# Optimization experiments

Hardware: AMD Instinct MI355X
Metric: run time of the kernel (lower is better)

Reference implementation:

```python
import jax, jax.numpy as jnp
import numpy as np

D_MODEL = 1024
N_HEAD = 16
ATT_DIM = D_MODEL // N_HEAD


def setup_inputs() -> dict:
    key = jax.random.key(0)
    ks = jax.random.split(key, 7)
    B, S = 2, 2048
    q = jax.random.normal(ks[0], (B, S, D_MODEL), dtype=jnp.float32)
    k = jax.random.normal(ks[1], (B, S, D_MODEL), dtype=jnp.float32)
    v = jax.random.normal(ks[2], (B, S, D_MODEL), dtype=jnp.float32)
    # per-head projection weights, stored as [H, d_model, att_dim] (x @ W form)
    scale_qkv = float(np.sqrt(6.0 / (D_MODEL + ATT_DIM)))  # xavier_uniform
    Wq = jax.random.uniform(ks[3], (N_HEAD, D_MODEL, ATT_DIM), jnp.float32, -scale_qkv, scale_qkv)
    Wk = jax.random.uniform(ks[4], (N_HEAD, D_MODEL, ATT_DIM), jnp.float32, -scale_qkv, scale_qkv)
    Wv = jax.random.uniform(ks[5], (N_HEAD, D_MODEL, ATT_DIM), jnp.float32, -scale_qkv, scale_qkv)
    scale_o = float(np.sqrt(6.0 / (D_MODEL + D_MODEL)))
    Wo = jax.random.uniform(ks[6], (D_MODEL, D_MODEL), jnp.float32, -scale_o, scale_o)
    return {"q": q, "k": k, "v": v, "Wq": Wq, "Wk": Wk, "Wv": Wv, "Wo": Wo}


def reference(q, k, v, Wq, Wk, Wv, Wo):
    # per-head projections, batched over heads: [H,B,S,E]
    qh = jnp.einsum('bsd,hde->hbse', q, Wq)
    kh = jnp.einsum('bsd,hde->hbse', k, Wk)
    vh = jnp.einsum('bsd,hde->hbse', v, Wv)
    # NOTE: original divides by att_dim (not sqrt(att_dim))
    scores = jnp.einsum('hbqe,hbke->hbqk', qh, kh) / ATT_DIM
    attn = jax.nn.softmax(scores, axis=-1)  # [H,B,Sq,Sk]
    att = jnp.einsum('hbqk,hbke->hbqe', attn, vh)  # [H,B,S,E]
    # concat heads along last dim in head order, then output projection
    H, B, S, E = att.shape
    cat = jnp.transpose(att, (1, 2, 0, 3)).reshape(B, S, H * E)
    out = cat @ Wo  # dropout is identity in eval
    return (out, attn)
```

## Files before the change

### kernel.cpp

```cpp
#include <hip/hip_runtime.h>
#include <hip/hip_bf16.h>

#define DM 1024
#define NH 16
#define AD 64
#define BB 2
#define SS 2048
#define LOG2E 1.44269504f

typedef float f32x4 __attribute__((ext_vector_type(4)));
typedef short bf16x8 __attribute__((ext_vector_type(8)));
typedef unsigned short u16;
typedef unsigned int u32;
typedef u16 u16x4 __attribute__((ext_vector_type(4)));
typedef u16 u16x8 __attribute__((ext_vector_type(8)));
typedef u32 u32x4 __attribute__((ext_vector_type(4)));

static __device__ __forceinline__ u16 f2bf(float f) {
  unsigned u = __builtin_bit_cast(unsigned, f);
  u += 0x7fffu + ((u >> 16) & 1u);
  return (u16)(u >> 16);
}

#define MFMA16(a, b, c) __builtin_amdgcn_mfma_f32_16x16x32_bf16((a), (b), (c), 0, 0, 0)

static __device__ __forceinline__ void ld_lds16(const void* g, void* l) {
  __builtin_amdgcn_global_load_lds((const __attribute__((address_space(1))) u32*)g,
                                   (__attribute__((address_space(3))) u32*)l, 16, 0, 0);
}

#define KFRAG(buf, row, P) (*(const bf16x8*)(&(buf)[(row) * 64 + ((((P) ^ ((row) & 7))) << 3)]))
#define V64(buf, row, P, hh) \
  (*(const u16x4*)(&(buf)[(row) * 64 + ((((P) ^ ((row) & 7))) << 3) + (hh) * 4]))

__global__ __launch_bounds__(256, 4) void cast_bf16_kernel(const float* __restrict__ src,
                                                           u16* __restrict__ dst, int n8) {
  int i = blockIdx.x * blockDim.x + threadIdx.x;
  int stride = gridDim.x * blockDim.x;
  for (; i < n8; i += stride) {
    const f32x4* p = (const f32x4*)src + 2 * (size_t)i;
    f32x4 a = p[0], b = p[1];
    u16x8 o;
    o[0] = f2bf(a[0]); o[1] = f2bf(a[1]); o[2] = f2bf(a[2]); o[3] = f2bf(a[3]);
    o[4] = f2bf(b[0]); o[5] = f2bf(b[1]); o[6] = f2bf(b[2]); o[7] = f2bf(b[3]);
    *((u16x8*)dst + i) = o;
  }
}

__global__ __launch_bounds__(256, 4) void tcast_kernel(const float* __restrict__ src,
                                                       u16* __restrict__ dst, int R, int C,
                                                       float scale) {
  __shared__ float T[64][65];
  long bo = (long)blockIdx.z * R * C;
  int r0 = blockIdx.x * 64, c0 = blockIdx.y * 64;
  int cl = threadIdx.x & 63, rl = threadIdx.x >> 6;
#pragma unroll
  for (int i = 0; i < 16; i++) {
    int rr = rl + 4 * i;
    T[cl][rr] = src[bo + (long)(r0 + rr) * C + c0 + cl];
  }
  __syncthreads();
#pragma unroll
  for (int i = 0; i < 16; i++) {
    int cc = rl + 4 * i;
    dst[bo + (long)(c0 + cc) * R + r0 + cl] = f2bf(T[cc][cl] * scale);
  }
}

template <int MODE>
__global__ __launch_bounds__(256, 5) void proj_kernel(const u16* __restrict__ X,
                                                      const u16* __restrict__ WT,
                                                      void* __restrict__ outp, long ob, long oh,
                                                      long os, long oe) {
  __shared__ u16 Ab[2][64 * 64];
  __shared__ u16 Bb[2][64 * 64];
  int s0 = blockIdx.x * 64, h = blockIdx.y, b = blockIdx.z;
  int tid = threadIdx.x, w = tid >> 6, lane = tid & 63, g = lane >> 4, li = lane & 15;
  const u16* xb = X + ((long)b * SS + s0) * DM;
  const u16* wb = WT + (long)h * 64 * DM;
  int r1 = tid >> 3, p1 = (tid ^ (r1 & 7)) & 7;
  int r2 = (tid + 256) >> 3, p2 = ((tid + 256) ^ (r2 & 7)) & 7;
  const u16* as1 = xb + (long)r1 * DM + p1 * 8;
  const u16* as2 = xb + (long)r2 * DM + p2 * 8;
  const u16* bs1 = wb + (long)r1 * DM + p1 * 8;
  const u16* bs2 = wb + (long)r2 * DM + p2 * 8;
  u16* ad0 = &Ab[0][tid * 8]; u16* ad0b = &Ab[0][(tid + 256) * 8];
  u16* ad1 = &Ab[1][tid * 8]; u16* ad1b = &Ab[1][(tid + 256) * 8];
  u16* bd0 = &Bb[0][tid * 8]; u16* bd0b = &Bb[0][(tid + 256) * 8];
  u16* bd1 = &Bb[1][tid * 8]; u16* bd1b = &Bb[1][(tid + 256) * 8];

  ld_lds16(as1, ad0); ld_lds16(as2, ad0b);
  ld_lds16(bs1, bd0); ld_lds16(bs2, bd0b);
  asm volatile("s_waitcnt vmcnt(0)" ::: "memory");
  __syncthreads();

  f32x4 acc[4] = {};
  for (int kc = 0; kc < DM / 64; kc++) {
    if (kc + 1 < DM / 64) {
      int ko = (kc + 1) * 64;
      if (kc & 1) {
        ld_lds16(as1 + ko, ad0); ld_lds16(as2 + ko, ad0b);
        ld_lds16(bs1 + ko, bd0); ld_lds16(bs2 + ko, bd0b);
      } else {
        ld_lds16(as1 + ko, ad1); ld_lds16(as2 + ko, ad1b);
        ld_lds16(bs1 + ko, bd1); ld_lds16(bs2 + ko, bd1b);
      }
    }
    const u16* ab = Ab[kc & 1];
    const u16* bbuf = Bb[kc & 1];
    bf16x8 bf0 = KFRAG(bbuf, w * 16 + li, g);
    bf16x8 bf1 = KFRAG(bbuf, w * 16 + li, 4 + g);
#pragma unroll
    for (int mi = 0; mi < 4; mi++) {
      bf16x8 a0 = KFRAG(ab, mi * 16 + li, g);
      bf16x8 a1 = KFRAG(ab, mi * 16 + li, 4 + g);
      acc[mi] = MFMA16(a0, bf0, acc[mi]);
      acc[mi] = MFMA16(a1, bf1, acc[mi]);
    }
    asm volatile("s_waitcnt vmcnt(0)" ::: "memory");
    __syncthreads();
  }

  int e = w * 16 + li;
  long bh = (long)b * ob + (long)h * oh;
#pragma unroll
  for (int mi = 0; mi < 4; mi++) {
    int sb = s0 + mi * 16 + 4 * g;
    if (MODE == 0) {
      u16* o = (u16*)outp;
#pragma unroll
      for (int r = 0; r < 4; r++) o[bh + (long)(sb + r) * os + (long)e * oe] = f2bf(acc[mi][r]);
    } else if (MODE == 1) {
      u16x4 v;
#pragma unroll
      for (int r = 0; r < 4; r++) v[r] = f2bf(acc[mi][r]);
      *(u16x4*)((u16*)outp + bh + (long)e * oe + sb) = v;
    } else {
      float* o = (float*)outp;
#pragma unroll
      for (int r = 0; r < 4; r++) o[bh + (long)(sb + r) * os + (long)e * oe] = acc[mi][r];
    }
  }
}

__global__ __launch_bounds__(512, 4) void attn_kernel(const u16* __restrict__ qh,
                                                      const u16* __restrict__ kh,
                                                      const u16* __restrict__ vhT,
                                                      float* __restrict__ attn_out,
                                                      u16* __restrict__ cat) {
  __shared__ u16 Kb[2][64 * 64];
  __shared__ u16 Vb[2][64 * 64];
  int h = blockIdx.y, b = blockIdx.z;
  int hb = h * BB + b;
  int tid = threadIdx.x;
  int w = tid >> 6, lane = tid & 63;
  int g = lane >> 4, li = lane & 15;
  long base = (long)hb * SS * AD;
  const u16* qhb = qh + base;
  const u16* khb = kh + base;
  const u16* vhb = vhT + base;
  int q0 = blockIdx.x * 128 + w * 16;

  bf16x8 bq0 = *(const bf16x8*)(qhb + (q0 + li) * AD + 8 * g);
  bf16x8 bq1 = *(const bf16x8*)(qhb + (q0 + li) * AD + 32 + 8 * g);

  int srow = tid >> 3, spiece = (tid ^ (srow & 7)) & 7;
  const u16* ksrc = khb + (long)srow * AD + spiece * 8;
  const u16* vsrc = vhb + (long)srow * SS + spiece * 8;
  u16* kd0 = &Kb[0][tid * 8]; u16* kd1 = &Kb[1][tid * 8];
  u16* vd0 = &Vb[0][tid * 8]; u16* vd1 = &Vb[1][tid * 8];

  float m_run = -3.0e38f, l_run = 0.f;
  ld_lds16(ksrc, kd0);
  asm volatile("s_waitcnt vmcnt(0)" ::: "memory");
  __syncthreads();
  for (int ch = 0; ch < SS / 64; ch++) {
    if (ch + 1 < SS / 64) ld_lds16(ksrc + (ch + 1) * 64 * AD, (ch & 1) ? kd0 : kd1);
    const u16* kb = Kb[ch & 1];
    f32x4 sacc[4] = {};
#pragma unroll
    for (int mi = 0; mi < 4; mi++) {
      bf16x8 a0 = KFRAG(kb, mi * 16 + li, g);
      bf16x8 a1 = KFRAG(kb, mi * 16 + li, 4 + g);
      sacc[mi] = MFMA16(a0, bq0, sacc[mi]);
      sacc[mi] = MFMA16(a1, bq1, sacc[mi]);
    }
    float cm = m_run;
#pragma unroll
    for (int c = 0; c < 4; c++)
#pragma unroll
      for (int r = 0; r < 4; r++) cm = fmaxf(cm, sacc[c][r]);
    l_run *= exp2f((m_run - cm) * LOG2E);
#pragma unroll
    for (int c = 0; c < 4; c++)
#pragma unroll
      for (int r = 0; r < 4; r++) l_run += exp2f((sacc[c][r] - cm) * LOG2E);
    m_run = cm;
    asm volatile("s_waitcnt vmcnt(0)" ::: "memory");
    __syncthreads();
  }
#pragma unroll
  for (int d = 16; d <= 32; d <<= 1) {
    float om = __shfl_xor(m_run, d);
    float ol = __shfl_xor(l_run, d);
    float nm = fmaxf(m_run, om);
    l_run = l_run * exp2f((m_run - nm) * LOG2E) + ol * exp2f((om - nm) * LOG2E);
    m_run = nm;
  }
  float rinv = 1.0f / l_run;
  float mC = m_run * LOG2E;

  ld_lds16(ksrc, kd0);
  ld_lds16(vsrc, vd0);
  asm volatile("s_waitcnt vmcnt(0)" ::: "memory");
  __syncthreads();
  f32x4 accv[4] = {};
  float* arow = attn_out + ((long)hb * SS + q0 + li) * SS;
  for (int ch = 0; ch < SS / 64; ch++) {
    if (ch + 1 < SS / 64) {
      ld_lds16(ksrc + (ch + 1) * 64 * AD, (ch & 1) ? kd0 : kd1);
      ld_lds16(vsrc + (ch + 1) * 64, (ch & 1) ? vd0 : vd1);
    }
    const u16* kb = Kb[ch & 1];
    const u16* vb = Vb[ch & 1];
    f32x4 sacc[4] = {};
#pragma unroll
    for (int mi = 0; mi < 4; mi++) {
      bf16x8 a0 = KFRAG(kb, mi * 16 + li, g);
      bf16x8 a1 = KFRAG(kb, mi * 16 + li, 4 + g);
      sacc[mi] = MFMA16(a0, bq0, sacc[mi]);
      sacc[mi] = MFMA16(a1, bq1, sacc[mi]);
    }
    u32 pw[8];
#pragma unroll
    for (int c = 0; c < 4; c++) {
      f32x4 pv;
#pragma unroll
      for (int r = 0; r < 4; r++) pv[r] = exp2f(sacc[c][r] * LOG2E - mC) * rinv;
      *(f32x4*)(arow + ch * 64 + c * 16 + 4 * g) = pv;
      pw[2 * c] = (u32)f2bf(pv[0]) | ((u32)f2bf(pv[1]) << 16);
      pw[2 * c + 1] = (u32)f2bf(pv[2]) | ((u32)f2bf(pv[3]) << 16);
    }
#pragma unroll
    for (int kk = 0; kk < 2; kk++) {
      u32x4 aw = {pw[4 * kk], pw[4 * kk + 1], pw[4 * kk + 2], pw[4 * kk + 3]};
      bf16x8 ap = __builtin_bit_cast(bf16x8, aw);
#pragma unroll
      for (int et = 0; et < 4; et++) {
        int row = et * 16 + li;
        u16x4 b0 = V64(vb, row, 4 * kk + (g >> 1), g & 1);
        u16x4 b1 = V64(vb, row, 4 * kk + 2 + (g >> 1), g & 1);
        u16x8 ub = {b0[0], b0[1], b0[2], b0[3], b1[0], b1[1], b1[2], b1[3]};
        bf16x8 bv = __builtin_bit_cast(bf16x8, ub);
        accv[et] = MFMA16(ap, bv, accv[et]);
      }
    }
    asm volatile("s_waitcnt vmcnt(0)" ::: "memory");
    __syncthreads();
  }

#pragma unroll
  for (int et = 0; et < 4; et++)
#pragma unroll
    for (int r = 0; r < 4; r++)
      cat[((long)b * SS + q0 + 4 * g + r) * DM + h * AD + et * 16 + li] = f2bf(accv[et][r]);
}

extern "C" void kernel_launch(void* const* d_in, const int* in_sizes, int n_in, void* d_out,
                              int out_size, void* d_ws, size_t ws_size, hipStream_t stream) {
  const float* q = (const float*)d_in[0];
  const float* k = (const float*)d_in[1];
  const float* v = (const float*)d_in[2];
  const float* Wq = (const float*)d_in[3];
  const float* Wk = (const float*)d_in[4];
  const float* Wv = (const float*)d_in[5];
  const float* Wo = (const float*)d_in[6];
  float* out = (float*)d_out;
  float* attn_out = out + (long)BB * SS * DM;

  const long NX = (long)BB * SS * DM;
  const long NW = (long)NH * DM * AD;
  u16* ws = (u16*)d_ws;
  u16* xq = ws;
  u16* xk = xq + NX;
  u16* xv = xk + NX;
  u16* WqT = xv + NX;
  u16* WkT = WqT + NW;
  u16* WvT = WkT + NW;
  u16* WoT = WvT + NW;
  u16* qhw = WoT + (long)DM * DM;
  u16* khw = qhw + NX;
  u16* vhw = khw + NX;
  u16* catw = vhw + NX;

  cast_bf16_kernel<<<2048, 256, 0, stream>>>(q, xq, (int)(NX / 8));
  cast_bf16_kernel<<<2048, 256, 0, stream>>>(k, xk, (int)(NX / 8));
  cast_bf16_kernel<<<2048, 256, 0, stream>>>(v, xv, (int)(NX / 8));
  tcast_kernel<<<dim3(16, 1, NH), 256, 0, stream>>>(Wq, WqT, DM, AD, 1.0f / AD);
  tcast_kernel<<<dim3(16, 1, NH), 256, 0, stream>>>(Wk, WkT, DM, AD, 1.0f);
  tcast_kernel<<<dim3(16, 1, NH), 256, 0, stream>>>(Wv, WvT, DM, AD, 1.0f);
  tcast_kernel<<<dim3(16, 16, 1), 256, 0, stream>>>(Wo, WoT, DM, DM, 1.0f);

  dim3 pg(SS / 64, NH, BB);
  proj_kernel<0><<<pg, 256, 0, stream>>>(xq, WqT, qhw, (long)SS * AD, (long)BB * SS * AD, AD, 1);
  proj_kernel<0><<<pg, 256, 0, stream>>>(xk, WkT, khw, (long)SS * AD, (long)BB * SS * AD, AD, 1);
  proj_kernel<1><<<pg, 256, 0, stream>>>(xv, WvT, vhw, (long)SS * AD, (long)BB * SS * AD, 1, SS);

  attn_kernel<<<dim3(SS / 128, NH, BB), 512, 0, stream>>>(qhw, khw, vhw, attn_out, catw);

  proj_kernel<2><<<pg, 256, 0, stream>>>(catw, WoT, out, (long)SS * DM, AD, DM, 1);
}
```

Baseline: 305.3 us.

## Overlap async LDS prefetch with compute via partial vmcnt waits; merge cast launches

Replaces the full vmcnt(0) wait at the end of each loop iteration with a partial wait placed before the barrier at the top of the loop, so the next tile's global-to-LDS load stays in flight while the current tile is computed. This applies to the projection kernel and both attention passes. It also folds the softmax normalisation into the exponent offset (log2 of the row sum) and merges the three activation casts and three weight transposes into single launches to cut launch overhead. The hand-counted vmcnt values must match the number of outstanding loads, including the attn_out stores in the second attention pass, or the kernel can read stale LDS data.

```diff
diff --git a/kernel.cpp b/kernel.cpp
--- a/kernel.cpp
+++ b/kernel.cpp
@@ -29,12 +29,29 @@
                                    (__attribute__((address_space(3))) u32*)l, 16, 0, 0);
 }
 
+#define WAITV(N)                                             \
+  do {                                                       \
+    asm volatile("s_waitcnt vmcnt(" #N ")" ::: "memory");    \
+    __builtin_amdgcn_sched_barrier(0);                       \
+  } while (0)
+#define WAITL0()                                             \
+  do {                                                       \
+    asm volatile("s_waitcnt lgkmcnt(0)" ::: "memory");       \
+    __builtin_amdgcn_sched_barrier(0);                       \
+  } while (0)
+#define BAR() __builtin_amdgcn_s_barrier()
+
 #define KFRAG(buf, row, P) (*(const bf16x8*)(&(buf)[(row) * 64 + ((((P) ^ ((row) & 7))) << 3)]))
 #define V64(buf, row, P, hh) \
   (*(const u16x4*)(&(buf)[(row) * 64 + ((((P) ^ ((row) & 7))) << 3) + (hh) * 4]))
 
-__global__ __launch_bounds__(256, 4) void cast_bf16_kernel(const float* __restrict__ src,
-                                                           u16* __restrict__ dst, int n8) {
+__global__ __launch_bounds__(256, 4) void cast3_kernel(const float* __restrict__ s0,
+                                                       const float* __restrict__ s1,
+                                                       const float* __restrict__ s2,
+                                                       u16* __restrict__ d0, u16* __restrict__ d1,
+                                                       u16* __restrict__ d2, int n8) {
+  const float* src = blockIdx.y == 0 ? s0 : blockIdx.y == 1 ? s1 : s2;
+  u16* dst = blockIdx.y == 0 ? d0 : blockIdx.y == 1 ? d1 : d2;
   int i = blockIdx.x * blockDim.x + threadIdx.x;
   int stride = gridDim.x * blockDim.x;
   for (; i < n8; i += stride) {
@@ -47,11 +64,26 @@
   }
 }
 
-__global__ __launch_bounds__(256, 4) void tcast_kernel(const float* __restrict__ src,
+template <int MODE>
+__global__ __launch_bounds__(256, 4) void tcast_kernel(const float* __restrict__ s0,
+                                                       const float* __restrict__ s1,
+                                                       const float* __restrict__ s2,
                                                        u16* __restrict__ dst, int R, int C,
-                                                       float scale) {
+                                                       float scale0) {
   __shared__ float T[64][65];
-  long bo = (long)blockIdx.z * R * C;
+  const float* src;
+  u16* dstp;
+  float scale;
+  long bo;
+  if (MODE == 0) {
+    src = s0; bo = (long)blockIdx.z * R * C; dstp = dst; scale = scale0;
+  } else {
+    int which = blockIdx.z >> 4, zz = blockIdx.z & 15;
+    src = which == 0 ? s0 : which == 1 ? s1 : s2;
+    bo = (long)zz * R * C;
+    dstp = dst + (long)which * NH * R * C;
+    scale = which == 0 ? scale0 : 1.0f;
+  }
   int r0 = blockIdx.x * 64, c0 = blockIdx.y * 64;
   int cl = threadIdx.x & 63, rl = threadIdx.x >> 6;
 #pragma unroll
@@ -63,7 +95,7 @@
 #pragma unroll
   for (int i = 0; i < 16; i++) {
     int cc = rl + 4 * i;
-    dst[bo + (long)(c0 + cc) * R + r0 + cl] = f2bf(T[cc][cl] * scale);
+    dstp[bo + (long)(c0 + cc) * R + r0 + cl] = f2bf(T[cc][cl] * scale);
   }
 }
 
@@ -91,8 +123,6 @@
 
   ld_lds16(as1, ad0); ld_lds16(as2, ad0b);
   ld_lds16(bs1, bd0); ld_lds16(bs2, bd0b);
-  asm volatile("s_waitcnt vmcnt(0)" ::: "memory");
-  __syncthreads();
 
   f32x4 acc[4] = {};
   for (int kc = 0; kc < DM / 64; kc++) {
@@ -105,7 +135,11 @@
         ld_lds16(as1 + ko, ad1); ld_lds16(as2 + ko, ad1b);
         ld_lds16(bs1 + ko, bd1); ld_lds16(bs2 + ko, bd1b);
       }
-    }
+      WAITV(4);
+    } else {
+      WAITV(0);
+    }
+    BAR();
     const u16* ab = Ab[kc & 1];
     const u16* bbuf = Bb[kc & 1];
     bf16x8 bf0 = KFRAG(bbuf, w * 16 + li, g);
@@ -117,8 +151,8 @@
       acc[mi] = MFMA16(a0, bf0, acc[mi]);
       acc[mi] = MFMA16(a1, bf1, acc[mi]);
     }
-    asm volatile("s_waitcnt vmcnt(0)" ::: "memory");
-    __syncthreads();
+    WAITL0();
+    BAR();
   }
 
   int e = w * 16 + li;
@@ -172,10 +206,14 @@
 
   float m_run = -3.0e38f, l_run = 0.f;
   ld_lds16(ksrc, kd0);
-  asm volatile("s_waitcnt vmcnt(0)" ::: "memory");
-  __syncthreads();
   for (int ch = 0; ch < SS / 64; ch++) {
-    if (ch + 1 < SS / 64) ld_lds16(ksrc + (ch + 1) * 64 * AD, (ch & 1) ? kd0 : kd1);
+    if (ch + 1 < SS / 64) {
+      ld_lds16(ksrc + (ch + 1) * 64 * AD, (ch & 1) ? kd0 : kd1);
+      WAITV(1);
+    } else {
+      WAITV(0);
+    }
+    BAR();
     const u16* kb = Kb[ch & 1];
     f32x4 sacc[4] = {};
 #pragma unroll
@@ -196,8 +234,8 @@
 #pragma unroll
       for (int r = 0; r < 4; r++) l_run += exp2f((sacc[c][r] - cm) * LOG2E);
     m_run = cm;
-    asm volatile("s_waitcnt vmcnt(0)" ::: "memory");
-    __syncthreads();
+    WAITL0();
+    BAR();
   }
 #pragma unroll
   for (int d = 16; d <= 32; d <<= 1) {
@@ -207,20 +245,25 @@
     l_run = l_run * exp2f((m_run - nm) * LOG2E) + ol * exp2f((om - nm) * LOG2E);
     m_run = nm;
   }
-  float rinv = 1.0f / l_run;
-  float mC = m_run * LOG2E;
+  float moff = m_run * LOG2E + log2f(l_run);
 
   ld_lds16(ksrc, kd0);
   ld_lds16(vsrc, vd0);
-  asm volatile("s_waitcnt vmcnt(0)" ::: "memory");
-  __syncthreads();
   f32x4 accv[4] = {};
   float* arow = attn_out + ((long)hb * SS + q0 + li) * SS;
   for (int ch = 0; ch < SS / 64; ch++) {
     if (ch + 1 < SS / 64) {
       ld_lds16(ksrc + (ch + 1) * 64 * AD, (ch & 1) ? kd0 : kd1);
       ld_lds16(vsrc + (ch + 1) * 64, (ch & 1) ? vd0 : vd1);
-    }
+      if (ch == 0) {
+        WAITV(2);
+      } else {
+        WAITV(6);
+      }
+    } else {
+      WAITV(4);
+    }
+    BAR();
     const u16* kb = Kb[ch & 1];
     const u16* vb = Vb[ch & 1];
     f32x4 sacc[4] = {};
@@ -236,7 +279,7 @@
     for (int c = 0; c < 4; c++) {
       f32x4 pv;
 #pragma unroll
-      for (int r = 0; r < 4; r++) pv[r] = exp2f(sacc[c][r] * LOG2E - mC) * rinv;
+      for (int r = 0; r < 4; r++) pv[r] = exp2f(sacc[c][r] * LOG2E - moff);
       *(f32x4*)(arow + ch * 64 + c * 16 + 4 * g) = pv;
       pw[2 * c] = (u32)f2bf(pv[0]) | ((u32)f2bf(pv[1]) << 16);
       pw[2 * c + 1] = (u32)f2bf(pv[2]) | ((u32)f2bf(pv[3]) << 16);
@@ -255,8 +298,8 @@
         accv[et] = MFMA16(ap, bv, accv[et]);
       }
     }
-    asm volatile("s_waitcnt vmcnt(0)" ::: "memory");
-    __syncthreads();
+    WAITL0();
+    BAR();
   }
 
 #pragma unroll
@@ -293,13 +336,9 @@
   u16* vhw = khw + NX;
   u16* catw = vhw + NX;
 
-  cast_bf16_kernel<<<2048, 256, 0, stream>>>(q, xq, (int)(NX / 8));
-  cast_bf16_kernel<<<2048, 256, 0, stream>>>(k, xk, (int)(NX / 8));
-  cast_bf16_kernel<<<2048, 256, 0, stream>>>(v, xv, (int)(NX / 8));
-  tcast_kernel<<<dim3(16, 1, NH), 256, 0, stream>>>(Wq, WqT, DM, AD, 1.0f / AD);
-  tcast_kernel<<<dim3(16, 1, NH), 256, 0, stream>>>(Wk, WkT, DM, AD, 1.0f);
-  tcast_kernel<<<dim3(16, 1, NH), 256, 0, stream>>>(Wv, WvT, DM, AD, 1.0f);
-  tcast_kernel<<<dim3(16, 16, 1), 256, 0, stream>>>(Wo, WoT, DM, DM, 1.0f);
+  cast3_kernel<<<dim3(700, 3), 256, 0, stream>>>(q, k, v, xq, xk, xv, (int)(NX / 8));
+  tcast_kernel<1><<<dim3(16, 1, 48), 256, 0, stream>>>(Wq, Wk, Wv, WqT, DM, AD, 1.0f / AD);
+  tcast_kernel<0><<<dim3(16, 16, 1), 256, 0, stream>>>(Wo, nullptr, nullptr, WoT, DM, DM, 1.0f);
 
   dim3 pg(SS / 64, NH, BB);
   proj_kernel<0><<<pg, 256, 0, stream>>>(xq, WqT, qhw, (long)SS * AD, (long)BB * SS * AD, AD, 1);
```

Result: faster. 282.0 us (-7.6%).
